# Kernel tuning notes

Hardware: AMD Instinct MI355X
Metric: run time of the kernel (lower is better)

The kernel has to match this reference:

```python
import jax, jax.numpy as jnp
import numpy as np

B, N, D, H = 128, 32, 256, 1024

def setup_inputs() -> dict:
    key = jax.random.key(0)
    k1, k2, k3, k4, k5 = jax.random.split(key, 5)
    attribute_embeddings = jax.random.normal(k1, (B, N, D), dtype=jnp.float32)
    # MLP params: Linear(D->H), ReLU, Linear(H->D). Kaiming-uniform-ish init scale.
    W1 = jax.random.normal(k2, (D, H), dtype=jnp.float32) * (1.0 / np.sqrt(D))
    b1 = jax.random.normal(k3, (H,), dtype=jnp.float32) * 0.01
    W2 = jax.random.normal(k4, (H, D), dtype=jnp.float32) * (1.0 / np.sqrt(H))
    b2 = jax.random.normal(k5, (D,), dtype=jnp.float32) * 0.01
    return {"attribute_embeddings": attribute_embeddings, "W1": W1, "b1": b1, "W2": W2, "b2": b2}

def reference(attribute_embeddings, W1, b1, W2, b2):
    x = attribute_embeddings  # [B, N, D]
    # All pairwise elementwise products: [B, N, N, D]
    pair = x[:, :, None, :] * x[:, None, :, :]
    # Batched 2-layer MLP over the last dim
    h = jax.nn.relu(jnp.einsum('bijd,dh->bijh', pair, W1) + b1)  # [B, N, N, H]
    out = jnp.einsum('bijh,hd->bijd', h, W2) + b2                # [B, N, N, D]
    # Original sums over dim=1 (the i index) -> [B, N, D]
    return jnp.sum(out, axis=1)
```

## Files before the change

kernel.cpp:

```cpp
#include <hip/hip_runtime.h>

typedef __attribute__((ext_vector_type(8))) _Float16 f16x8;
typedef __attribute__((ext_vector_type(4))) _Float16 f16x4;
typedef __attribute__((ext_vector_type(4))) float f32x4;

typedef __attribute__((address_space(3))) unsigned int lds_u32;
typedef const __attribute__((address_space(1))) unsigned int g_u32;

#define DEV_INLINE __device__ __forceinline__

constexpr int B_ = 128, N_ = 32, D_ = 256, H_ = 1024;
constexpr int XPAD = 260;
constexpr int SROW = 1032;

constexpr int LDS_MAIN = 102656;

DEV_INLINE void gload_lds16(const void* g, void* l) {
    __builtin_amdgcn_global_load_lds((g_u32*)g, (lds_u32*)l, 16, 0, 0);
}

#define BARRIER() asm volatile("s_barrier" ::: "memory")

__global__ void prep2(const float* __restrict__ W1, const float* __restrict__ W2,
                      _Float16* __restrict__ W1T, _Float16* __restrict__ W2T) {
    __shared__ float tile[32][36];
    const int t = threadIdx.x;
    const int r = t >> 3, cq = (t & 7) * 4;
    int bb = blockIdx.x;
    if (bb < 256) {
        int tk = bb >> 5, th = bb & 31;
        *(f32x4*)&tile[r][cq] = *(const f32x4*)(W1 + (size_t)(tk * 32 + r) * 1024 + th * 32 + cq);
        __syncthreads();
        f16x4 o;
        #pragma unroll
        for (int q = 0; q < 4; ++q) o[q] = (_Float16)tile[cq + q][r];
        *(f16x4*)(W1T + (size_t)(th * 32 + r) * 256 + tk * 32 + cq) = o;
    } else {
        bb -= 256;
        int th = bb >> 3, td = bb & 7;
        *(f32x4*)&tile[r][cq] = *(const f32x4*)(W2 + (size_t)(th * 32 + r) * 256 + td * 32 + cq);
        __syncthreads();
        f16x4 o;
        #pragma unroll
        for (int q = 0; q < 4; ++q) o[q] = (_Float16)tile[cq + q][r];
        *(f16x4*)(W2T + (size_t)(td * 32 + r) * 1024 + th * 32 + cq) = o;
    }
}

__global__ __launch_bounds__(512, 2)
void interaction_main(const float* __restrict__ Xg, const float* __restrict__ b1g,
                      const float* __restrict__ b2g, const _Float16* __restrict__ W1T,
                      const _Float16* __restrict__ W2T, float* __restrict__ outg) {
    __shared__ __align__(16) unsigned char smem[LDS_MAIN];

    const int tid = threadIdx.x;
    const int w = tid >> 6, l = tid & 63, l15 = l & 15, lg = l >> 4;
    const int bid = blockIdx.x;
    const int b = bid >> 1, jg = bid & 1;
    const int j0 = jg * 16;

    float*     Xs  = (float*)smem;
    _Float16*  s16 = (_Float16*)(smem + 65536);
    float*     b1s = (float*)(smem + 98560);

    {
        const float* xb = Xg + (size_t)b * (N_ * D_);
        int row = tid >> 4, c0 = (tid & 15) * 16;
        #pragma unroll
        for (int q = 0; q < 4; ++q)
            *(f32x4*)(Xs + row * XPAD + c0 + q * 4) = *(const f32x4*)(xb + row * 256 + c0 + q * 4);
        b1s[tid]       = b1g[tid];
        b1s[tid + 512] = b1g[tid + 512];
    }
    __syncthreads();

    f16x8 afrag[2][2][8];
    {
        const float* xja = Xs + (j0 + w) * XPAD;
        const float* xjb = Xs + (j0 + 8 + w) * XPAD;
        #pragma unroll
        for (int ks = 0; ks < 8; ++ks) {
            int k0 = ks * 32 + lg * 8;
            f32x4 jA0 = *(const f32x4*)(xja + k0);
            f32x4 jA1 = *(const f32x4*)(xja + k0 + 4);
            f32x4 jB0 = *(const f32x4*)(xjb + k0);
            f32x4 jB1 = *(const f32x4*)(xjb + k0 + 4);
            #pragma unroll
            for (int rt = 0; rt < 2; ++rt) {
                const float* xi = Xs + (rt * 16 + l15) * XPAD + k0;
                f32x4 x0 = *(const f32x4*)(xi);
                f32x4 x1 = *(const f32x4*)(xi + 4);
                f16x8 a, c;
                a[0] = (_Float16)(x0[0] * jA0[0]); c[0] = (_Float16)(x0[0] * jB0[0]);
                a[1] = (_Float16)(x0[1] * jA0[1]); c[1] = (_Float16)(x0[1] * jB0[1]);
                a[2] = (_Float16)(x0[2] * jA0[2]); c[2] = (_Float16)(x0[2] * jB0[2]);
                a[3] = (_Float16)(x0[3] * jA0[3]); c[3] = (_Float16)(x0[3] * jB0[3]);
                a[4] = (_Float16)(x1[0] * jA1[0]); c[4] = (_Float16)(x1[0] * jB1[0]);
                a[5] = (_Float16)(x1[1] * jA1[1]); c[5] = (_Float16)(x1[1] * jB1[1]);
                a[6] = (_Float16)(x1[2] * jA1[2]); c[6] = (_Float16)(x1[2] * jB1[2]);
                a[7] = (_Float16)(x1[3] * jA1[3]); c[7] = (_Float16)(x1[3] * jB1[3]);
                afrag[0][rt][ks] = a;
                afrag[1][rt][ks] = c;
            }
        }
    }
    __syncthreads();

    auto stage = [&](int c) {
        const int bufbase = (c & 1) * 32768;
        #pragma unroll
        for (int p = 0; p < 4; ++p) {
            int hc   = ((p * 8 + w) << 1) + (l >> 5);
            int srco = ((l & 31) ^ (hc & 7)) << 3;
            const _Float16* src = W1T + (size_t)(c * 64 + hc) * 256 + srco;
            void* dst = smem + bufbase + (p * 8 + w) * 1024;
            gload_lds16(src, dst);
        }
    };

    stage(0);

    for (int c = 0; c < 16; ++c) {
        if (c < 15) {
            stage(c + 1);
            asm volatile("s_waitcnt vmcnt(4)" ::: "memory");
        } else {
            asm volatile("s_waitcnt vmcnt(0)" ::: "memory");
        }
        BARRIER();

        const int bufbase = (c & 1) * 32768;
        f32x4 acc[2][2][4] = {};
        __builtin_amdgcn_s_setprio(1);
        #pragma unroll
        for (int ks = 0; ks < 8; ++ks) {
            #pragma unroll
            for (int ct = 0; ct < 4; ++ct) {
                int hc = ct * 16 + l15;
                int boff = bufbase + hc * 512 + ((ks * 64 + lg * 16) ^ ((hc & 7) << 4));
                f16x8 bfr = *(const f16x8*)(smem + boff);
                acc[0][0][ct] = __builtin_amdgcn_mfma_f32_16x16x32_f16(afrag[0][0][ks], bfr, acc[0][0][ct], 0, 0, 0);
                acc[0][1][ct] = __builtin_amdgcn_mfma_f32_16x16x32_f16(afrag[0][1][ks], bfr, acc[0][1][ct], 0, 0, 0);
                acc[1][0][ct] = __builtin_amdgcn_mfma_f32_16x16x32_f16(afrag[1][0][ks], bfr, acc[1][0][ct], 0, 0, 0);
                acc[1][1][ct] = __builtin_amdgcn_mfma_f32_16x16x32_f16(afrag[1][1][ks], bfr, acc[1][1][ct], 0, 0, 0);
            }
        }
        __builtin_amdgcn_s_setprio(0);

        #pragma unroll
        for (int ct = 0; ct < 4; ++ct) {
            int hcol = c * 64 + ct * 16 + l15;
            float bv = b1s[hcol];
            float v0 = 0.f, v1 = 0.f;
            #pragma unroll
            for (int rt = 0; rt < 2; ++rt)
                #pragma unroll
                for (int r = 0; r < 4; ++r) {
                    v0 += fmaxf(acc[0][rt][ct][r] + bv, 0.f);
                    v1 += fmaxf(acc[1][rt][ct][r] + bv, 0.f);
                }
            v0 += __shfl_xor(v0, 16, 64);
            v0 += __shfl_xor(v0, 32, 64);
            v1 += __shfl_xor(v1, 16, 64);
            v1 += __shfl_xor(v1, 32, 64);
            if (lg < 2) {
                int row = w + (lg << 3);
                s16[row * SROW + hcol] = (_Float16)(lg ? v1 : v0);
            }
        }
        BARRIER();
    }

    __syncthreads();

    f32x4 acc2[2] = {};
    #pragma unroll
    for (int ks = 0; ks < 32; ++ks) {
        f16x8 af = *(const f16x8*)(s16 + l15 * SROW + ks * 32 + lg * 8);
        #pragma unroll
        for (int t2 = 0; t2 < 2; ++t2) {
            const _Float16* bp = W2T + (size_t)((w * 2 + t2) * 16 + l15) * 1024 + ks * 32 + lg * 8;
            f16x8 bf = *(const f16x8*)bp;
            acc2[t2] = __builtin_amdgcn_mfma_f32_16x16x32_f16(af, bf, acc2[t2], 0, 0, 0);
        }
    }
    #pragma unroll
    for (int t2 = 0; t2 < 2; ++t2) {
        int d = (w * 2 + t2) * 16 + l15;
        float bb = 32.f * b2g[d];
        #pragma unroll
        for (int r = 0; r < 4; ++r) {
            int jloc = lg * 4 + r;
            outg[(size_t)(b * 32 + j0 + jloc) * 256 + d] = acc2[t2][r] + bb;
        }
    }
}

extern "C" void kernel_launch(void* const* d_in, const int* in_sizes, int n_in,
                              void* d_out, int out_size, void* d_ws, size_t ws_size,
                              hipStream_t stream) {
    const float* X  = (const float*)d_in[0];
    const float* W1 = (const float*)d_in[1];
    const float* b1 = (const float*)d_in[2];
    const float* W2 = (const float*)d_in[3];
    const float* b2 = (const float*)d_in[4];
    float* out = (float*)d_out;

    _Float16* W1T = (_Float16*)d_ws;
    _Float16* W2T = W1T + 262144;

    prep2<<<dim3(512), dim3(256), 0, stream>>>(W1, W2, W1T, W2T);
    interaction_main<<<dim3(B_ * (N_ / 16)), dim3(512), 0, stream>>>(X, b1, b2, W1T, W2T, out);
}
```

Baseline: 136.3 us.

## Hold W1 fragments in registers per wave and loop over j pairs

Each wave now keeps a 64-column slice of W1 in registers, loaded directly from global memory, and loops over the 16 j rows. The pairwise products are formed in fp16 on the fly from cached xi and xj fragments, so the double-buffered LDS staging of W1 with its barriers goes away. LDS use shrinks enough that more blocks could fit per CU. In exchange, register pressure rises sharply (64 f16x8 W1 fragments plus 16 xi fragments), the products lose some precision because they are computed in fp16, and each block rereads W1 from global or L2.

```diff
diff --git a/kernel.cpp b/kernel.cpp
--- a/kernel.cpp
+++ b/kernel.cpp
@@ -4,22 +4,12 @@
 typedef __attribute__((ext_vector_type(4))) _Float16 f16x4;
 typedef __attribute__((ext_vector_type(4))) float f32x4;
 
-typedef __attribute__((address_space(3))) unsigned int lds_u32;
-typedef const __attribute__((address_space(1))) unsigned int g_u32;
+constexpr int B_ = 128, N_ = 32, D_ = 256, H_ = 1024;
+constexpr int XPAD  = 260;
+constexpr int SROW  = 1032;
+constexpr int XJROW = 264;
 
-#define DEV_INLINE __device__ __forceinline__
-
-constexpr int B_ = 128, N_ = 32, D_ = 256, H_ = 1024;
-constexpr int XPAD = 260;
-constexpr int SROW = 1032;
-
-constexpr int LDS_MAIN = 102656;
-
-DEV_INLINE void gload_lds16(const void* g, void* l) {
-    __builtin_amdgcn_global_load_lds((g_u32*)g, (lds_u32*)l, 16, 0, 0);
-}
-
-#define BARRIER() asm volatile("s_barrier" ::: "memory")
+constexpr int LDS_MAIN = 45824;
 
 __global__ void prep2(const float* __restrict__ W1, const float* __restrict__ W2,
                       _Float16* __restrict__ W1T, _Float16* __restrict__ W2T) {
@@ -59,9 +49,10 @@
     const int b = bid >> 1, jg = bid & 1;
     const int j0 = jg * 16;
 
-    float*     Xs  = (float*)smem;
-    _Float16*  s16 = (_Float16*)(smem + 65536);
-    float*     b1s = (float*)(smem + 98560);
+    float*     Xs   = (float*)smem;
+    _Float16*  s16  = (_Float16*)smem;
+    _Float16*  xj16 = (_Float16*)(smem + 33280);
+    float*     b1s  = (float*)(smem + 41728);
 
     {
         const float* xb = Xg + (size_t)b * (N_ * D_);
@@ -74,119 +65,86 @@
     }
     __syncthreads();
 
-    f16x8 afrag[2][2][8];
     {
-        const float* xja = Xs + (j0 + w) * XPAD;
-        const float* xjb = Xs + (j0 + 8 + w) * XPAD;
+        int row = tid >> 5, c8 = (tid & 31) * 8;
+        const float* src = Xs + (j0 + row) * XPAD + c8;
+        f16x8 o;
+        #pragma unroll
+        for (int q = 0; q < 8; ++q) o[q] = (_Float16)src[q];
+        *(f16x8*)(xj16 + row * XJROW + c8) = o;
+    }
+
+    f16x8 xi16[2][8];
+    #pragma unroll
+    for (int nt = 0; nt < 2; ++nt)
         #pragma unroll
         for (int ks = 0; ks < 8; ++ks) {
-            int k0 = ks * 32 + lg * 8;
-            f32x4 jA0 = *(const f32x4*)(xja + k0);
-            f32x4 jA1 = *(const f32x4*)(xja + k0 + 4);
-            f32x4 jB0 = *(const f32x4*)(xjb + k0);
-            f32x4 jB1 = *(const f32x4*)(xjb + k0 + 4);
+            const float* src = Xs + (nt * 16 + l15) * XPAD + ks * 32 + lg * 8;
+            f16x8 o;
             #pragma unroll
-            for (int rt = 0; rt < 2; ++rt) {
-                const float* xi = Xs + (rt * 16 + l15) * XPAD + k0;
-                f32x4 x0 = *(const f32x4*)(xi);
-                f32x4 x1 = *(const f32x4*)(xi + 4);
-                f16x8 a, c;
-                a[0] = (_Float16)(x0[0] * jA0[0]); c[0] = (_Float16)(x0[0] * jB0[0]);
-                a[1] = (_Float16)(x0[1] * jA0[1]); c[1] = (_Float16)(x0[1] * jB0[1]);
-                a[2] = (_Float16)(x0[2] * jA0[2]); c[2] = (_Float16)(x0[2] * jB0[2]);
-                a[3] = (_Float16)(x0[3] * jA0[3]); c[3] = (_Float16)(x0[3] * jB0[3]);
-                a[4] = (_Float16)(x1[0] * jA1[0]); c[4] = (_Float16)(x1[0] * jB1[0]);
-                a[5] = (_Float16)(x1[1] * jA1[1]); c[5] = (_Float16)(x1[1] * jB1[1]);
-                a[6] = (_Float16)(x1[2] * jA1[2]); c[6] = (_Float16)(x1[2] * jB1[2]);
-                a[7] = (_Float16)(x1[3] * jA1[3]); c[7] = (_Float16)(x1[3] * jB1[3]);
-                afrag[0][rt][ks] = a;
-                afrag[1][rt][ks] = c;
+            for (int q = 0; q < 8; ++q) o[q] = (_Float16)src[q];
+            xi16[nt][ks] = o;
+        }
+    __syncthreads();
+
+    for (int hg = 0; hg < 2; ++hg) {
+        const int hbase = hg * 512 + w * 64;
+
+        f16x8 w1f[4][8];
+        #pragma unroll
+        for (int ct = 0; ct < 4; ++ct) {
+            const _Float16* wp = W1T + (size_t)(hbase + ct * 16 + l15) * 256 + lg * 8;
+            #pragma unroll
+            for (int ks = 0; ks < 8; ++ks)
+                w1f[ct][ks] = *(const f16x8*)(wp + ks * 32);
+        }
+        float b1v[4];
+        #pragma unroll
+        for (int ct = 0; ct < 4; ++ct) b1v[ct] = b1s[hbase + ct * 16 + l15];
+
+        for (int j = 0; j < 16; ++j) {
+            const _Float16* xjp = xj16 + j * XJROW + lg * 8;
+            f32x4 acc[2][4] = {};
+            #pragma unroll
+            for (int ks = 0; ks < 8; ++ks) {
+                f16x8 xjf = *(const f16x8*)(xjp + ks * 32);
+                f16x8 p0 = xi16[0][ks] * xjf;
+                f16x8 p1 = xi16[1][ks] * xjf;
+                #pragma unroll
+                for (int ct = 0; ct < 4; ++ct) {
+                    acc[0][ct] = __builtin_amdgcn_mfma_f32_16x16x32_f16(p0, w1f[ct][ks], acc[0][ct], 0, 0, 0);
+                    acc[1][ct] = __builtin_amdgcn_mfma_f32_16x16x32_f16(p1, w1f[ct][ks], acc[1][ct], 0, 0, 0);
+                }
+            }
+            #pragma unroll
+            for (int ct = 0; ct < 4; ++ct) {
+                float v = 0.f;
+                #pragma unroll
+                for (int nt = 0; nt < 2; ++nt)
+                    #pragma unroll
+                    for (int r = 0; r < 4; ++r)
+                        v += fmaxf(acc[nt][ct][r] + b1v[ct], 0.f);
+                v += __shfl_xor(v, 16, 64);
+                v += __shfl_xor(v, 32, 64);
+                if (l < 16) s16[j * SROW + hbase + ct * 16 + l15] = (_Float16)v;
             }
         }
     }
     __syncthreads();
 
-    auto stage = [&](int c) {
-        const int bufbase = (c & 1) * 32768;
-        #pragma unroll
-        for (int p = 0; p < 4; ++p) {
-            int hc   = ((p * 8 + w) << 1) + (l >> 5);
-            int srco = ((l & 31) ^ (hc & 7)) << 3;
-            const _Float16* src = W1T + (size_t)(c * 64 + hc) * 256 + srco;
-            void* dst = smem + bufbase + (p * 8 + w) * 1024;
-            gload_lds16(src, dst);
-        }
-    };
-
-    stage(0);
-
-    for (int c = 0; c < 16; ++c) {
-        if (c < 15) {
-            stage(c + 1);
-            asm volatile("s_waitcnt vmcnt(4)" ::: "memory");
-        } else {
-            asm volatile("s_waitcnt vmcnt(0)" ::: "memory");
-        }
-        BARRIER();
-
-        const int bufbase = (c & 1) * 32768;
-        f32x4 acc[2][2][4] = {};
-        __builtin_amdgcn_s_setprio(1);
-        #pragma unroll
-        for (int ks = 0; ks < 8; ++ks) {
-            #pragma unroll
-            for (int ct = 0; ct < 4; ++ct) {
-                int hc = ct * 16 + l15;
-                int boff = bufbase + hc * 512 + ((ks * 64 + lg * 16) ^ ((hc & 7) << 4));
-                f16x8 bfr = *(const f16x8*)(smem + boff);
-                acc[0][0][ct] = __builtin_amdgcn_mfma_f32_16x16x32_f16(afrag[0][0][ks], bfr, acc[0][0][ct], 0, 0, 0);
-                acc[0][1][ct] = __builtin_amdgcn_mfma_f32_16x16x32_f16(afrag[0][1][ks], bfr, acc[0][1][ct], 0, 0, 0);
-                acc[1][0][ct] = __builtin_amdgcn_mfma_f32_16x16x32_f16(afrag[1][0][ks], bfr, acc[1][0][ct], 0, 0, 0);
-                acc[1][1][ct] = __builtin_amdgcn_mfma_f32_16x16x32_f16(afrag[1][1][ks], bfr, acc[1][1][ct], 0, 0, 0);
-            }
-        }
-        __builtin_amdgcn_s_setprio(0);
-
-        #pragma unroll
-        for (int ct = 0; ct < 4; ++ct) {
-            int hcol = c * 64 + ct * 16 + l15;
-            float bv = b1s[hcol];
-            float v0 = 0.f, v1 = 0.f;
-            #pragma unroll
-            for (int rt = 0; rt < 2; ++rt)
-                #pragma unroll
-                for (int r = 0; r < 4; ++r) {
-                    v0 += fmaxf(acc[0][rt][ct][r] + bv, 0.f);
-                    v1 += fmaxf(acc[1][rt][ct][r] + bv, 0.f);
-                }
-            v0 += __shfl_xor(v0, 16, 64);
-            v0 += __shfl_xor(v0, 32, 64);
-            v1 += __shfl_xor(v1, 16, 64);
-            v1 += __shfl_xor(v1, 32, 64);
-            if (lg < 2) {
-                int row = w + (lg << 3);
-                s16[row * SROW + hcol] = (_Float16)(lg ? v1 : v0);
-            }
-        }
-        BARRIER();
-    }
-
-    __syncthreads();
-
     f32x4 acc2[2] = {};
-    #pragma unroll
+    const _Float16* ap  = s16 + l15 * SROW + lg * 8;
+    const _Float16* bp0 = W2T + (size_t)(w * 32 + l15) * 1024 + lg * 8;
+    const _Float16* bp1 = bp0 + 16 * 1024;
+    #pragma unroll 8
     for (int ks = 0; ks < 32; ++ks) {
-        f16x8 af = *(const f16x8*)(s16 + l15 * SROW + ks * 32 + lg * 8);
-        #pragma unroll
-        for (int t2 = 0; t2 < 2; ++t2) {
-            const _Float16* bp = W2T + (size_t)((w * 2 + t2) * 16 + l15) * 1024 + ks * 32 + lg * 8;
-            f16x8 bf = *(const f16x8*)bp;
-            acc2[t2] = __builtin_amdgcn_mfma_f32_16x16x32_f16(af, bf, acc2[t2], 0, 0, 0);
-        }
+        f16x8 af = *(const f16x8*)(ap + ks * 32);
+        acc2[0] = __builtin_amdgcn_mfma_f32_16x16x32_f16(af, *(const f16x8*)(bp0 + ks * 32), acc2[0], 0, 0, 0);
+        acc2[1] = __builtin_amdgcn_mfma_f32_16x16x32_f16(af, *(const f16x8*)(bp1 + ks * 32), acc2[1], 0, 0, 0);
     }
     #pragma unroll
     for (int t2 = 0; t2 < 2; ++t2) {
-        int d = (w * 2 + t2) * 16 + l15;
+        int d = w * 32 + t2 * 16 + l15;
         float bb = 32.f * b2g[d];
         #pragma unroll
         for (int r = 0; r < 4; ++r) {
@@ -210,5 +168,5 @@
     _Float16* W2T = W1T + 262144;
 
     prep2<<<dim3(512), dim3(256), 0, stream>>>(W1, W2, W1T, W2T);
-    interaction_main<<<dim3(B_ * (N_ / 16)), dim3(512), 0, stream>>>(X, b1, b2, W1T, W2T, out);
+    interaction_main<<<dim3(B_ * 2), dim3(512), 0, stream>>>(X, b1, b2, W1T, W2T, out);
 }
```

New measurement: 177.4 us. 30.1% more time.
